# Performance work log

Measured on AMD Instinct MI355X. Metric: run time of the kernel, lower is better.

Reference implementation:

```python
import jax, jax.numpy as jnp
import numpy as np

N = 20000   # nodes per type (lnc and dis)
E = 160000  # edges per meta-path graph and per pos/neg link graph
H = 8       # attention heads
D = 32      # out_size per head (H*D = 256 flattened)
HID = 256   # hidden_size from ResNet projection


def _bn(x, g, b, eps=1e-5):
    # training-mode BatchNorm1d (biased variance, like torch)
    m = x.mean(0)
    v = x.var(0)
    return g * (x - m) * jax.lax.rsqrt(v + eps) + b


def _leaky(x, slope):
    return jnp.where(x >= 0, x, slope * x)


def _gat(h_src, h_dst, src, dst, W, al, ar, n_dst):
    # DGL GATConv (bipartite, shared fc, no bias, eval mode)
    fs = (h_src @ W).reshape(-1, H, D)          # [Ns,H,D]
    fd = (h_dst @ W).reshape(-1, H, D)          # [Nd,H,D]
    el = (fs * al).sum(-1)                      # [Ns,H]
    er = (fd * ar).sum(-1)                      # [Nd,H]
    e = _leaky(el[src] + er[dst], 0.2)          # [E,H]
    emax = jax.ops.segment_max(e, dst, num_segments=n_dst)
    emax = jnp.where(jnp.isfinite(emax), emax, 0.0)   # zero in-degree safety
    ee = jnp.exp(e - emax[dst])
    den = jax.ops.segment_sum(ee, dst, num_segments=n_dst)
    a = ee / jnp.maximum(den[dst], 1e-9)        # edge softmax over incoming edges
    out = jax.ops.segment_sum(a[:, :, None] * fs[src], dst, num_segments=n_dst)
    return _leaky(out, 0.01).reshape(n_dst, H * D)  # activation=F.leaky_relu, flatten(1)


def _sem_attn(z, W1, b1, w2):
    # z: [N, 2, H*D]; SemanticAttention
    w = (jnp.tanh(z @ W1 + b1) @ w2).mean(0)    # [2]
    beta = jax.nn.softmax(w, axis=0)            # [2]
    return (beta[None, :, None] * z).sum(1)     # [N, H*D]


def setup_inputs() -> dict:
    key = jax.random.key(0)
    ks = jax.random.split(key, 32)
    s = 0.05
    inp = {
        "x_lnc": jax.random.normal(ks[0], (N, 256), jnp.float32),
        "x_dis": jax.random.normal(ks[1], (N, 256), jnp.float32),
        "proj_W": jax.random.normal(ks[2], (2, 256, HID), jnp.float32) * s,
        "proj_bn_g": jnp.ones((HID,), jnp.float32),
        "proj_bn_b": jnp.zeros((HID,), jnp.float32),
        "short_W": jax.random.normal(ks[3], (2, 256, HID), jnp.float32) * s,
        "short_b": jnp.zeros((2, HID), jnp.float32),
        "gat_W": jax.random.normal(ks[4], (4, HID, H * D), jnp.float32) * s,
        "gat_al": jax.random.normal(ks[5], (4, H, D), jnp.float32) * s,
        "gat_ar": jax.random.normal(ks[6], (4, H, D), jnp.float32) * s,
        "sem_W1": jax.random.normal(ks[7], (H * D, 128), jnp.float32) * s,
        "sem_b1": jnp.zeros((128,), jnp.float32),
        "sem_w2": jax.random.normal(ks[8], (128,), jnp.float32) * s,
    }
    names = ["ld_src", "ld_dst", "ll_src", "ll_dst", "dl_src", "dl_dst",
             "dd_src", "dd_dst", "pos_src", "pos_dst", "neg_src", "neg_dst"]
    for i, nm in enumerate(names):
        inp[nm] = jax.random.randint(ks[10 + i], (E,), 0, N, jnp.int32)
    return inp


def reference(x_lnc, x_dis, proj_W, proj_bn_g, proj_bn_b, short_W, short_b,
              gat_W, gat_al, gat_ar, sem_W1, sem_b1, sem_w2,
              ld_src, ld_dst, ll_src, ll_dst, dl_src, dl_dst,
              dd_src, dd_dst, pos_src, pos_dst, neg_src, neg_dst):
    # ResNet projection (shared BN applied per-branch, training-mode stats)
    l_x = _leaky(_bn(x_lnc @ proj_W[0], proj_bn_g, proj_bn_b), 0.01) + (x_lnc @ short_W[0] + short_b[0])
    d_x = _leaky(_bn(x_dis @ proj_W[1], proj_bn_g, proj_bn_b), 0.01) + (x_dis @ short_W[1] + short_b[1])
    # HANLayer: 4 meta-path GATs with pairings (l,d),(l,l),(d,l),(d,d)
    e0 = _gat(l_x, d_x, ld_src, ld_dst, gat_W[0], gat_al[0], gat_ar[0], N)  # dst dis
    e1 = _gat(l_x, l_x, ll_src, ll_dst, gat_W[1], gat_al[1], gat_ar[1], N)  # dst lnc
    e2 = _gat(d_x, l_x, dl_src, dl_dst, gat_W[2], gat_al[2], gat_ar[2], N)  # dst lnc
    e3 = _gat(d_x, d_x, dd_src, dd_dst, gat_W[3], gat_al[3], gat_ar[3], N)  # dst dis
    l_embs = _sem_attn(jnp.stack((e1, e2), axis=1), sem_W1, sem_b1, sem_w2)
    d_embs = _sem_attn(jnp.stack((e0, e3), axis=1), sem_W1, sem_b1, sem_w2)
    # Hadamard u_mul_v over 'lnc-dis' edges (pos graph and neg graph)
    pos_z = l_embs[pos_src] * d_embs[pos_dst]
    neg_z = l_embs[neg_src] * d_embs[neg_dst]
    return pos_z, neg_z, l_embs, d_embs
```

## Files before the change

kernel.cpp:

```cpp
#include <hip/hip_runtime.h>
#include <math.h>

#define NN 20000
#define NE 160000
#define SLOT 40

typedef _Float16 f16;
typedef __attribute__((ext_vector_type(8))) _Float16 f16x8;
typedef __attribute__((ext_vector_type(4))) float f32x4;

__device__ __forceinline__ float leakyf(float x, float s){ return x >= 0.f ? x : s*x; }
__device__ __forceinline__ ushort f2h(float x){ f16 h = (f16)x; ushort u; __builtin_memcpy(&u,&h,2); return u; }
__device__ __forceinline__ float h2f(ushort u){ f16 h; __builtin_memcpy(&h,&u,2); return (float)h; }

__device__ __forceinline__ void gload_lds16(const void* g, void* l){
  __builtin_amdgcn_global_load_lds((const __attribute__((address_space(1))) uint*)g,
                                   (__attribute__((address_space(3))) uint*)l, 16, 0, 0);
}

__global__ __launch_bounds__(256) void prep(const float* __restrict__ x_lnc,
    const float* __restrict__ x_dis, const float* __restrict__ proj_W,
    const float* __restrict__ short_W, const float* __restrict__ gat_W,
    const float* __restrict__ gat_al, const float* __restrict__ gat_ar,
    const float* __restrict__ sem_W1,
    ushort* __restrict__ xhl, ushort* __restrict__ xhd,
    ushort* btpl, ushort* btpd, ushort* btgl, ushort* btgd, ushort* btsm,
    int* __restrict__ zbuf){
  int b = blockIdx.x;
  if (b < 10000){
    const float* in = (b >= 5000) ? x_dis : x_lnc;
    ushort* out = (b >= 5000) ? xhd : xhl;
    long idx = (long)(b % 5000)*256 + threadIdx.x;
    long r = idx>>6; int c4 = (int)(idx&63)<<2;
    float4 v = *(const float4*)(in + r*256 + c4);
    ushort4 o; o.x=f2h(v.x); o.y=f2h(v.y); o.z=f2h(v.z); o.w=f2h(v.w);
    *(ushort4*)(out + r*256 + c4) = o;
  } else if (b < 12688){
    int idx = (b-10000)*256 + threadIdx.x;
    float v; ushort* out; int n, k;
    if (idx < 131072){
      n = idx>>8; k = idx&255; out = btpl;
      v = (n<256)? proj_W[(size_t)k*256+n] : short_W[(size_t)k*256+(n-256)];
    } else if (idx < 262144){
      int l = idx-131072; n = l>>8; k = l&255; out = btpd;
      v = (n<256)? proj_W[65536+(size_t)k*256+n] : short_W[65536+(size_t)k*256+(n-256)];
    } else if (idx < 458752){
      int l = idx-262144; n = l>>8; k = l&255; out = btgl;
      int sl = n>>8; const float* bb = gat_W + (sl==0?0:(sl==1?65536:131072));
      v = bb[(size_t)k*256 + (n&255)];
    } else if (idx < 655360){
      int l = idx-458752; n = l>>8; k = l&255; out = btgd;
      int sl = n>>8; const float* bb = gat_W + (sl==0?0:(sl==1?131072:196608));
      v = bb[(size_t)k*256 + (n&255)];
    } else {
      int l = idx-655360; n = l>>8; k = l&255; out = btsm;
      v = sem_W1[(size_t)k*128 + n];
    }
    out[(size_t)n*256 + k] = f2h(v);
  } else if (b < 12752){
    int idx = (b-12688)*256 + threadIdx.x;
    int side = idx >> 13;
    int r = idx & 8191;
    int c = r >> 8;
    int k = r & 255;
    int h = c & 7, sel = c >> 3;
    int gi; const float* av;
    if (side==0){
      gi = (sel==0)?0:((sel==3)?2:1);
      av = (sel<=1)? gat_al : gat_ar;
    } else {
      gi = (sel==0)?0:((sel==1)?2:3);
      av = (sel==1||sel==2)? gat_al : gat_ar;
    }
    const float* wrow = gat_W + gi*65536 + (size_t)k*256 + h*32;
    const float* a = av + gi*256 + h*32;
    float s = 0.f;
    #pragma unroll
    for (int d=0; d<32; d++) s += wrow[d]*a[d];
    ushort* out = side ? btgd : btgl;
    out[(size_t)(768+c)*256 + k] = f2h(s);
  } else if (b < 12848){
    int idx = (b-12752)*256 + threadIdx.x;
    uint* pl = (uint*)(btgl + 800*256);
    uint* pd = (uint*)(btgd + 800*256);
    if (idx < 12288) pl[idx] = 0; else pd[idx-12288] = 0;
  } else {
    int idx = (b-12848)*256 + threadIdx.x;
    if (idx < 81028) zbuf[idx] = 0;
  }
}

__global__ void scatter_slots(const int* s0, const int* s1, const int* s2, const int* s3,
    const int* d0, const int* d1, const int* d2, const int* d3,
    int* __restrict__ cnt, int* __restrict__ slots){
  int g = blockIdx.y;
  const int* src = (g==0)?s0:(g==1)?s1:(g==2)?s2:s3;
  const int* dst = (g==0)?d0:(g==1)?d1:(g==2)?d2:d3;
  int i = blockIdx.x*256 + threadIdx.x;
  if (i<NE){
    int d = dst[i];
    int p = atomicAdd(&cnt[g*NN + d], 1);
    slots[(size_t)(g*NN + d)*SLOT + p] = src[i];
  }
}

template<int EPI>
__global__ __launch_bounds__(256) void gemm16(
    const ushort* __restrict__ A0, const ushort* __restrict__ A1,
    const ushort* __restrict__ B0, const ushort* __restrict__ B1,
    ushort* __restrict__ C0, ushort* __restrict__ C1, int ldc, int M,
    float* __restrict__ sbuf,
    float* __restrict__ elr_l, float* __restrict__ elr_d,
    const float* __restrict__ b1v, const float* __restrict__ w2v){
  const int z = blockIdx.z;
  const ushort* A = z ? A1 : A0;
  const ushort* Bt = z ? B1 : B0;
  ushort* C = z ? C1 : C0;
  __shared__ ushort sm[16384];
  char* smc = (char*)sm;
  const int tid = threadIdx.x;
  const int lane = tid & 63, wid = tid >> 6;
  const int wr = wid >> 1, wc = wid & 1;
  const int fr = lane & 15, fq = lane >> 4;
  const int brow = blockIdx.y*128, bcol = blockIdx.x*128;
  f32x4 acc[4][4];
  #pragma unroll
  for (int i=0;i<4;i++)
    #pragma unroll
    for (int j=0;j<4;j++) acc[i][j] = (f32x4){0.f,0.f,0.f,0.f};

  for (int k0 = 0; k0 < 256; k0 += 64){
    __syncthreads();
    #pragma unroll
    for (int cc = 0; cc < 8; cc++){
      int c = wid*8 + cc;
      int ch = c & 15;
      int rel = ch*1024 + lane*16;
      int row = rel >> 7;
      int scb = (rel & 127) ^ ((row & 7) << 4);
      const char* src;
      if (c < 16){
        int gr = brow + row; gr = (gr < M) ? gr : (M-1);
        src = (const char*)A + (size_t)gr*512 + k0*2 + scb;
      } else {
        src = (const char*)Bt + (size_t)(bcol + row)*512 + k0*2 + scb;
      }
      gload_lds16(src, smc + ((c<16)?0:16384) + ch*1024);
    }
    __syncthreads();
    #pragma unroll
    for (int ks = 0; ks < 2; ks++){
      f16x8 af[4], bfr[4];
      #pragma unroll
      for (int i=0;i<4;i++){
        int r = wr*64 + i*16 + fr;
        int koff = ks*32 + fq*8;
        int aoff = ((r<<7) + koff*2) ^ ((r&7)<<4);
        af[i] = *(const f16x8*)(smc + aoff);
        int n = wc*64 + i*16 + fr;
        int boff = ((n<<7) + koff*2) ^ ((n&7)<<4);
        bfr[i] = *(const f16x8*)(smc + 16384 + boff);
      }
      #pragma unroll
      for (int i=0;i<4;i++)
        #pragma unroll
        for (int j=0;j<4;j++)
          acc[i][j] = __builtin_amdgcn_mfma_f32_16x16x32_f16(af[i], bfr[j], acc[i][j], 0,0,0);
    }
  }

  if (EPI==1 || (EPI==2 && bcol < 768)){
    #pragma unroll
    for (int i=0;i<4;i++){
      #pragma unroll
      for (int e=0;e<4;e++){
        int gr = brow + wr*64 + i*16 + fq*4 + e;
        if (gr < M){
          #pragma unroll
          for (int j=0;j<4;j++)
            C[(size_t)gr*ldc + bcol + wc*64 + j*16 + fr] = f2h(acc[i][j][e]);
        }
      }
    }
  }

  if (EPI==2 && bcol >= 768 && wc == 0){
    float* elr = z ? elr_d : elr_l;
    #pragma unroll
    for (int i=0;i<4;i++){
      #pragma unroll
      for (int e=0;e<4;e++){
        int gr = brow + wr*64 + i*16 + fq*4 + e;
        if (gr < M){
          elr[(size_t)gr*32 + fr]      = acc[i][0][e];
          elr[(size_t)gr*32 + 16 + fr] = acc[i][1][e];
        }
      }
    }
  }

  if (EPI==1 && bcol < 256){
    float* gsum = sbuf + z*512;
    float* gsq  = gsum + 256;
    #pragma unroll
    for (int j=0;j<4;j++){
      float s=0.f, q=0.f;
      #pragma unroll
      for (int i=0;i<4;i++)
        #pragma unroll
        for (int e=0;e<4;e++){
          int gr = brow + wr*64 + i*16 + fq*4 + e;
          if (gr < M){ float v = acc[i][j][e]; s += v; q += v*v; }
        }
      s += __shfl_xor(s,16); s += __shfl_xor(s,32);
      q += __shfl_xor(q,16); q += __shfl_xor(q,32);
      if (fq==0){
        int gc = bcol + wc*64 + j*16 + fr;
        atomicAdd(&gsum[gc], s);
        atomicAdd(&gsq[gc], q);
      }
    }
  }

  if (EPI==3){
    float b1c[4], w2c[4];
    #pragma unroll
    for (int j=0;j<4;j++){
      int col = wc*64 + j*16 + fr;
      b1c[j] = b1v[col]; w2c[j] = w2v[col];
    }
    int segA = brow/20000;
    int bound = (segA+1)*20000;
    float t0=0.f, t1=0.f;
    #pragma unroll
    for (int i=0;i<4;i++){
      #pragma unroll
      for (int e=0;e<4;e++){
        int gr = brow + wr*64 + i*16 + fq*4 + e;
        float rs = 0.f;
        #pragma unroll
        for (int j=0;j<4;j++){
          float x = acc[i][j][e] + b1c[j];
          float ex = __expf(2.f*x);
          rs += (1.f - 2.f/(ex+1.f))*w2c[j];
        }
        if (gr < bound) t0 += rs; else t1 += rs;
      }
    }
    #pragma unroll
    for (int off=32; off>0; off>>=1){ t0 += __shfl_xor(t0,off); t1 += __shfl_xor(t1,off); }
    if (lane==0){
      atomicAdd(&sbuf[segA], t0);
      if (brow + 127 >= bound) atomicAdd(&sbuf[segA+1], t1);
    }
  }
}

__global__ __launch_bounds__(256) void proj_apply2(const ushort* __restrict__ PS_l,
    const ushort* __restrict__ PS_d, const float* __restrict__ sbuf,
    const float* __restrict__ gg, const float* __restrict__ bb,
    const float* __restrict__ short_b, ushort* __restrict__ out_l, ushort* __restrict__ out_d){
  int y = blockIdx.y;
  const ushort* PS = y ? PS_d : PS_l;
  ushort* out = y ? out_d : out_l;
  const float* gsum = sbuf + y*512;
  const float* gsq  = gsum + 256;
  const float* sb = short_b + y*256;
  long idx = (long)blockIdx.x*256 + threadIdx.x;
  long r = idx>>6; int c4 = (int)(idx&63)<<2;
  ushort4 pu = *(const ushort4*)(PS + r*512 + c4);
  ushort4 su = *(const ushort4*)(PS + r*512 + 256 + c4);
  float pv[4] = {h2f(pu.x),h2f(pu.y),h2f(pu.z),h2f(pu.w)};
  float sv[4] = {h2f(su.x),h2f(su.y),h2f(su.z),h2f(su.w)};
  ushort o[4];
  #pragma unroll
  for (int k=0;k<4;k++){
    int c = c4+k;
    float m = gsum[c]*(1.f/NN);
    float va = gsq[c]*(1.f/NN) - m*m;
    float ri = rsqrtf(va + 1e-5f);
    float yv = (pv[k]-m)*ri*gg[c] + bb[c];
    o[k] = f2h(leakyf(yv,0.01f) + sv[k] + sb[c]);
  }
  ushort4 ov; ov.x=o[0]; ov.y=o[1]; ov.z=o[2]; ov.w=o[3];
  *(ushort4*)(out + r*256 + c4) = ov;
}

__global__ __launch_bounds__(256) void gat_fused(const int* __restrict__ cnt,
    const int* __restrict__ slots, const float* __restrict__ elr_l,
    const float* __restrict__ elr_d, const ushort* __restrict__ fc_l,
    const ushort* __restrict__ fc_d, ushort* __restrict__ sems){
  const int g = blockIdx.y;
  const int n = blockIdx.x*4 + (threadIdx.x>>6);
  const int lane = threadIdx.x & 63;
  const int co[4]    = {0,256,256,512};
  const int semo[4]  = {40000,0,20000,60000};
  const int eloA[4]  = {0,8,8,16};
  const int eroA[4]  = {0,16,24,24};
  const float* elb = (g<2) ? elr_l : elr_d;
  const float* erb = (g==1||g==2) ? elr_l : elr_d;
  const int eloff = eloA[g], eroff = eroA[g];
  const ushort* F = (g<2) ? fc_l : fc_d;
  const int coloff = co[g];
  const int j = lane>>3, h = lane&7, hc = lane>>3;
  const int e1 = cnt[g*NN + n];
  const long sb = (long)(g*NN + n)*SLOT;
  const float ern = erb[(size_t)n*32 + eroff + h];
  float ssum = 0.f;
  float4 acc = make_float4(0.f,0.f,0.f,0.f);

  for (int base = 0; base < e1; base += 8){
    int idx = base + j;
    bool valid = idx < e1;
    int src = valid ? slots[sb + idx] : 0;
    float p = valid ? __expf(leakyf(elb[(size_t)src*32 + eloff + h] + ern, 0.2f)) : 0.f;
    ssum += p;
    #pragma unroll
    for (int e=0;e<8;e++){
      float w = __shfl(p, e*8 + hc);
      int s = __shfl(src, e*8);
      ushort4 fu = *(const ushort4*)(F + (size_t)s*768 + coloff + lane*4);
      acc.x = fmaf(w,h2f(fu.x),acc.x); acc.y = fmaf(w,h2f(fu.y),acc.y);
      acc.z = fmaf(w,h2f(fu.z),acc.z); acc.w = fmaf(w,h2f(fu.w),acc.w);
    }
  }
  ssum += __shfl_xor(ssum,8); ssum += __shfl_xor(ssum,16); ssum += __shfl_xor(ssum,32);
  float rd = 1.f/fmaxf(__shfl(ssum, hc), 1e-9f);
  ushort4 o;
  o.x = f2h(leakyf(acc.x*rd, 0.01f)); o.y = f2h(leakyf(acc.y*rd, 0.01f));
  o.z = f2h(leakyf(acc.z*rd, 0.01f)); o.w = f2h(leakyf(acc.w*rd, 0.01f));
  *(ushort4*)(sems + (size_t)(semo[g]+n)*256 + lane*4) = o;
}

__global__ __launch_bounds__(256) void sem_combine(const ushort* __restrict__ sems,
    const float* __restrict__ tsum, float* __restrict__ lemb, float* __restrict__ demb,
    ushort* __restrict__ lemb16, ushort* __restrict__ demb16){
  float wl0 = tsum[0]*(1.f/20000.f), wl1 = tsum[1]*(1.f/20000.f);
  float m = fmaxf(wl0,wl1);
  float ea = __expf(wl0-m), eb = __expf(wl1-m);
  float b0 = ea/(ea+eb), b1 = eb/(ea+eb);
  float wd0 = tsum[2]*(1.f/20000.f), wd1 = tsum[3]*(1.f/20000.f);
  m = fmaxf(wd0,wd1);
  ea = __expf(wd0-m); eb = __expf(wd1-m);
  float b2 = ea/(ea+eb), b3 = eb/(ea+eb);

  long idx = (long)blockIdx.x*256 + threadIdx.x;
  long r = idx>>6; int c4 = (int)(idx&63)<<2;
  ushort4 v1 = *(const ushort4*)(sems + (r          )*256 + c4);
  ushort4 v2 = *(const ushort4*)(sems + (r + 20000L )*256 + c4);
  ushort4 v0 = *(const ushort4*)(sems + (r + 40000L )*256 + c4);
  ushort4 v3 = *(const ushort4*)(sems + (r + 60000L )*256 + c4);
  float4 lo, dd;
  lo.x = b0*h2f(v1.x) + b1*h2f(v2.x); dd.x = b2*h2f(v0.x) + b3*h2f(v3.x);
  lo.y = b0*h2f(v1.y) + b1*h2f(v2.y); dd.y = b2*h2f(v0.y) + b3*h2f(v3.y);
  lo.z = b0*h2f(v1.z) + b1*h2f(v2.z); dd.z = b2*h2f(v0.z) + b3*h2f(v3.z);
  lo.w = b0*h2f(v1.w) + b1*h2f(v2.w); dd.w = b2*h2f(v0.w) + b3*h2f(v3.w);
  *(float4*)(lemb + r*256 + c4) = lo;
  *(float4*)(demb + r*256 + c4) = dd;
  ushort4 lh, dh;
  lh.x=f2h(lo.x); lh.y=f2h(lo.y); lh.z=f2h(lo.z); lh.w=f2h(lo.w);
  dh.x=f2h(dd.x); dh.y=f2h(dd.y); dh.z=f2h(dd.z); dh.w=f2h(dd.w);
  *(ushort4*)(lemb16 + r*256 + c4) = lh;
  *(ushort4*)(demb16 + r*256 + c4) = dh;
}

__global__ __launch_bounds__(256) void edge_mul2(const int* __restrict__ ps, const int* __restrict__ pd,
    const int* __restrict__ ns, const int* __restrict__ nd,
    const ushort* __restrict__ lemb16, const ushort* __restrict__ demb16,
    float* __restrict__ pos, float* __restrict__ neg){
  long idx = (long)blockIdx.x*256 + threadIdx.x;
  const long H = (long)NE*64;
  const int *es, *ed; float* out; long t;
  if (idx < H){ es=ps; ed=pd; out=pos; t=idx; }
  else { es=ns; ed=nd; out=neg; t=idx-H; }
  long i = t>>6; int jj = (int)(t&63);
  int s = es[i], d = ed[i];
  ushort4 a = *(const ushort4*)(lemb16 + (size_t)s*256 + (size_t)jj*4);
  ushort4 b = *(const ushort4*)(demb16 + (size_t)d*256 + (size_t)jj*4);
  float4 o = make_float4(h2f(a.x)*h2f(b.x), h2f(a.y)*h2f(b.y),
                         h2f(a.z)*h2f(b.z), h2f(a.w)*h2f(b.w));
  *(float4*)(out + (size_t)t*4) = o;
}

extern "C" void kernel_launch(void* const* d_in, const int* in_sizes, int n_in,
                              void* d_out, int out_size, void* d_ws, size_t ws_size,
                              hipStream_t stream){
  const float* x_lnc  = (const float*)d_in[0];
  const float* x_dis  = (const float*)d_in[1];
  const float* proj_W = (const float*)d_in[2];
  const float* bn_g   = (const float*)d_in[3];
  const float* bn_b   = (const float*)d_in[4];
  const float* short_W= (const float*)d_in[5];
  const float* short_b= (const float*)d_in[6];
  const float* gat_W  = (const float*)d_in[7];
  const float* gat_al = (const float*)d_in[8];
  const float* gat_ar = (const float*)d_in[9];
  const float* sem_W1 = (const float*)d_in[10];
  const float* sem_b1 = (const float*)d_in[11];
  const float* sem_w2 = (const float*)d_in[12];
  const int* g_src[4] = {(const int*)d_in[13],(const int*)d_in[15],(const int*)d_in[17],(const int*)d_in[19]};
  const int* g_dst[4] = {(const int*)d_in[14],(const int*)d_in[16],(const int*)d_in[18],(const int*)d_in[20]};
  const int* pos_src = (const int*)d_in[21];
  const int* pos_dst = (const int*)d_in[22];
  const int* neg_src = (const int*)d_in[23];
  const int* neg_dst = (const int*)d_in[24];

  const long LEMB = (long)NN*256;
  const long EOUT = (long)NE*256;

  float* outf = (float*)d_out;
  float* pos  = outf;
  float* negr = outf + EOUT;
  float* lemb = outf + 2*EOUT;
  float* demb = lemb + LEMB;

  ushort* PS_l = (ushort*)negr;
  ushort* PS_d = PS_l + 10240000;
  ushort* fc_l = (ushort*)negr;
  ushort* fc_d = fc_l + 15360000;

  float* ws   = (float*)d_ws;
  float* sbuf = ws;
  float* tsum = ws + 1024;
  int*   cnt  = (int*)(ws + 1028);
  float* elr_l = ws + 81028;
  float* elr_d = elr_l + 640000;
  int*   slots  = (int*)(elr_d + 640000);
  ushort* xhl  = (ushort*)(slots + 3200000);
  ushort* xhd  = xhl + 5120000;
  ushort* axl  = xhd + 5120000;
  ushort* axd  = axl + 5120000;
  ushort* sems = axd + 5120000;
  ushort* lemb16 = sems + 20480000;
  ushort* demb16 = lemb16 + 5120000;
  ushort* btpl = demb16 + 5120000;
  ushort* btpd = btpl + 131072;
  ushort* btgl = btpd + 131072;
  ushort* btgd = btgl + 229376;
  ushort* btsm = btgd + 229376;

  prep<<<13165,256,0,stream>>>(x_lnc, x_dis, proj_W, short_W, gat_W, gat_al, gat_ar,
                               sem_W1, xhl, xhd, btpl, btpd, btgl, btgd, btsm, (int*)ws);
  scatter_slots<<<dim3(625,4),256,0,stream>>>(g_src[0],g_src[1],g_src[2],g_src[3],
      g_dst[0],g_dst[1],g_dst[2],g_dst[3], cnt, slots);

  gemm16<1><<<dim3(4,157,2),256,0,stream>>>(xhl, xhd, btpl, btpd, PS_l, PS_d, 512, NN,
      sbuf, nullptr, nullptr, nullptr, nullptr);
  proj_apply2<<<dim3(5000,2),256,0,stream>>>(PS_l, PS_d, sbuf, bn_g, bn_b, short_b, axl, axd);

  gemm16<2><<<dim3(7,157,2),256,0,stream>>>(axl, axd, btgl, btgd, fc_l, fc_d, 768, NN,
      nullptr, elr_l, elr_d, nullptr, nullptr);

  gat_fused<<<dim3(5000,4),256,0,stream>>>(cnt, slots, elr_l, elr_d, fc_l, fc_d, sems);

  gemm16<3><<<dim3(1,625,1),256,0,stream>>>(sems, nullptr, btsm, nullptr, nullptr, nullptr, 128, 80000,
      tsum, nullptr, nullptr, sem_b1, sem_w2);

  sem_combine<<<5000,256,0,stream>>>(sems, tsum, lemb, demb, lemb16, demb16);

  edge_mul2<<<80000,256,0,stream>>>(pos_src, pos_dst, neg_src, neg_dst, lemb16, demb16, pos, negr);
}
```

Before: 386.7 us.

## Fold edge slot scatter into projection GEMM launch, tile weight transpose, nontemporal stores

```diff
diff --git a/kernel.cpp b/kernel.cpp
--- a/kernel.cpp
+++ b/kernel.cpp
@@ -16,6 +16,9 @@
 __device__ __forceinline__ void gload_lds16(const void* g, void* l){
   __builtin_amdgcn_global_load_lds((const __attribute__((address_space(1))) uint*)g,
                                    (__attribute__((address_space(3))) uint*)l, 16, 0, 0);
+}
+__device__ __forceinline__ void nts4(float* p, f32x4 v){
+  __builtin_nontemporal_store(v, (f32x4*)p);
 }
 
 __global__ __launch_bounds__(256) void prep(const float* __restrict__ x_lnc,
@@ -35,30 +38,45 @@
     float4 v = *(const float4*)(in + r*256 + c4);
     ushort4 o; o.x=f2h(v.x); o.y=f2h(v.y); o.z=f2h(v.z); o.w=f2h(v.w);
     *(ushort4*)(out + r*256 + c4) = o;
-  } else if (b < 12688){
-    int idx = (b-10000)*256 + threadIdx.x;
-    float v; ushort* out; int n, k;
-    if (idx < 131072){
-      n = idx>>8; k = idx&255; out = btpl;
-      v = (n<256)? proj_W[(size_t)k*256+n] : short_W[(size_t)k*256+(n-256)];
-    } else if (idx < 262144){
-      int l = idx-131072; n = l>>8; k = l&255; out = btpd;
-      v = (n<256)? proj_W[65536+(size_t)k*256+n] : short_W[65536+(size_t)k*256+(n-256)];
-    } else if (idx < 458752){
-      int l = idx-262144; n = l>>8; k = l&255; out = btgl;
-      int sl = n>>8; const float* bb = gat_W + (sl==0?0:(sl==1?65536:131072));
-      v = bb[(size_t)k*256 + (n&255)];
-    } else if (idx < 655360){
-      int l = idx-458752; n = l>>8; k = l&255; out = btgd;
-      int sl = n>>8; const float* bb = gat_W + (sl==0?0:(sl==1?131072:196608));
-      v = bb[(size_t)k*256 + (n&255)];
+  } else if (b < 10168){
+    int t = b - 10000;
+    const float* S; ushort* outb; int n0, k0, ldS=256, colbase;
+    if (t < 160){
+      int m = t >> 4, tt = t & 15;
+      n0 = (tt & 3) * 64; k0 = (tt >> 2) * 64;
+      switch(m){
+        case 0: S=proj_W;        outb=btpl; colbase=0;   break;
+        case 1: S=short_W;       outb=btpl; colbase=256; break;
+        case 2: S=proj_W+65536;  outb=btpd; colbase=0;   break;
+        case 3: S=short_W+65536; outb=btpd; colbase=256; break;
+        case 4: S=gat_W;         outb=btgl; colbase=0;   break;
+        case 5: S=gat_W+65536;   outb=btgl; colbase=256; break;
+        case 6: S=gat_W+131072;  outb=btgl; colbase=512; break;
+        case 7: S=gat_W;         outb=btgd; colbase=0;   break;
+        case 8: S=gat_W+131072;  outb=btgd; colbase=256; break;
+        default:S=gat_W+196608;  outb=btgd; colbase=512; break;
+      }
     } else {
-      int l = idx-655360; n = l>>8; k = l&255; out = btsm;
-      v = sem_W1[(size_t)k*128 + n];
-    }
-    out[(size_t)n*256 + k] = f2h(v);
-  } else if (b < 12752){
-    int idx = (b-12688)*256 + threadIdx.x;
+      int s = t - 160;
+      n0 = (s & 1)*64; k0 = (s >> 1)*64; ldS = 128;
+      S = sem_W1; outb = btsm; colbase = 0;
+    }
+    __shared__ float tile[64][65];
+    int tr = threadIdx.x >> 6;
+    int tc = threadIdx.x & 63;
+    #pragma unroll
+    for (int p=0;p<16;p++){
+      int kr = p*4 + tr;
+      tile[kr][tc] = S[(size_t)(k0+kr)*ldS + n0 + tc];
+    }
+    __syncthreads();
+    #pragma unroll
+    for (int p=0;p<16;p++){
+      int nr = p*4 + tr;
+      outb[(size_t)(colbase + n0 + nr)*256 + k0 + tc] = f2h(tile[tc][nr]);
+    }
+  } else if (b < 10232){
+    int idx = (b-10168)*256 + threadIdx.x;
     int side = idx >> 13;
     int r = idx & 8191;
     int c = r >> 8;
@@ -79,28 +97,14 @@
     for (int d=0; d<32; d++) s += wrow[d]*a[d];
     ushort* out = side ? btgd : btgl;
     out[(size_t)(768+c)*256 + k] = f2h(s);
-  } else if (b < 12848){
-    int idx = (b-12752)*256 + threadIdx.x;
+  } else if (b < 10328){
+    int idx = (b-10232)*256 + threadIdx.x;
     uint* pl = (uint*)(btgl + 800*256);
     uint* pd = (uint*)(btgd + 800*256);
     if (idx < 12288) pl[idx] = 0; else pd[idx-12288] = 0;
   } else {
-    int idx = (b-12848)*256 + threadIdx.x;
+    int idx = (b-10328)*256 + threadIdx.x;
     if (idx < 81028) zbuf[idx] = 0;
-  }
-}
-
-__global__ void scatter_slots(const int* s0, const int* s1, const int* s2, const int* s3,
-    const int* d0, const int* d1, const int* d2, const int* d3,
-    int* __restrict__ cnt, int* __restrict__ slots){
-  int g = blockIdx.y;
-  const int* src = (g==0)?s0:(g==1)?s1:(g==2)?s2:s3;
-  const int* dst = (g==0)?d0:(g==1)?d1:(g==2)?d2:d3;
-  int i = blockIdx.x*256 + threadIdx.x;
-  if (i<NE){
-    int d = dst[i];
-    int p = atomicAdd(&cnt[g*NN + d], 1);
-    slots[(size_t)(g*NN + d)*SLOT + p] = src[i];
   }
 }
 
@@ -111,8 +115,26 @@
     ushort* __restrict__ C0, ushort* __restrict__ C1, int ldc, int M,
     float* __restrict__ sbuf,
     float* __restrict__ elr_l, float* __restrict__ elr_d,
-    const float* __restrict__ b1v, const float* __restrict__ w2v){
+    const float* __restrict__ b1v, const float* __restrict__ w2v,
+    const int* s0, const int* s1, const int* s2, const int* s3,
+    const int* d0, const int* d1, const int* d2, const int* d3,
+    int* __restrict__ cnt, int* __restrict__ slots){
   const int z = blockIdx.z;
+  if (EPI==1 && z==2){
+    int bb = blockIdx.y*gridDim.x + blockIdx.x;
+    int tid = bb*256 + (int)threadIdx.x;
+    if (tid < NE){
+      #pragma unroll
+      for (int g=0; g<4; g++){
+        const int* src = (g==0)?s0:(g==1)?s1:(g==2)?s2:s3;
+        const int* dst = (g==0)?d0:(g==1)?d1:(g==2)?d2:d3;
+        int d = dst[tid];
+        int p = atomicAdd(&cnt[g*NN + d], 1);
+        slots[(size_t)(g*NN + d)*SLOT + p] = src[tid];
+      }
+    }
+    return;
+  }
   const ushort* A = z ? A1 : A0;
   const ushort* Bt = z ? B1 : B0;
   ushort* C = z ? C1 : C0;
@@ -350,16 +372,16 @@
   ushort4 v2 = *(const ushort4*)(sems + (r + 20000L )*256 + c4);
   ushort4 v0 = *(const ushort4*)(sems + (r + 40000L )*256 + c4);
   ushort4 v3 = *(const ushort4*)(sems + (r + 60000L )*256 + c4);
-  float4 lo, dd;
-  lo.x = b0*h2f(v1.x) + b1*h2f(v2.x); dd.x = b2*h2f(v0.x) + b3*h2f(v3.x);
-  lo.y = b0*h2f(v1.y) + b1*h2f(v2.y); dd.y = b2*h2f(v0.y) + b3*h2f(v3.y);
-  lo.z = b0*h2f(v1.z) + b1*h2f(v2.z); dd.z = b2*h2f(v0.z) + b3*h2f(v3.z);
-  lo.w = b0*h2f(v1.w) + b1*h2f(v2.w); dd.w = b2*h2f(v0.w) + b3*h2f(v3.w);
-  *(float4*)(lemb + r*256 + c4) = lo;
-  *(float4*)(demb + r*256 + c4) = dd;
+  f32x4 lo, dd;
+  lo[0] = b0*h2f(v1.x) + b1*h2f(v2.x); dd[0] = b2*h2f(v0.x) + b3*h2f(v3.x);
+  lo[1] = b0*h2f(v1.y) + b1*h2f(v2.y); dd[1] = b2*h2f(v0.y) + b3*h2f(v3.y);
+  lo[2] = b0*h2f(v1.z) + b1*h2f(v2.z); dd[2] = b2*h2f(v0.z) + b3*h2f(v3.z);
+  lo[3] = b0*h2f(v1.w) + b1*h2f(v2.w); dd[3] = b2*h2f(v0.w) + b3*h2f(v3.w);
+  nts4(lemb + r*256 + c4, lo);
+  nts4(demb + r*256 + c4, dd);
   ushort4 lh, dh;
-  lh.x=f2h(lo.x); lh.y=f2h(lo.y); lh.z=f2h(lo.z); lh.w=f2h(lo.w);
-  dh.x=f2h(dd.x); dh.y=f2h(dd.y); dh.z=f2h(dd.z); dh.w=f2h(dd.w);
+  lh.x=f2h(lo[0]); lh.y=f2h(lo[1]); lh.z=f2h(lo[2]); lh.w=f2h(lo[3]);
+  dh.x=f2h(dd[0]); dh.y=f2h(dd[1]); dh.z=f2h(dd[2]); dh.w=f2h(dd[3]);
   *(ushort4*)(lemb16 + r*256 + c4) = lh;
   *(ushort4*)(demb16 + r*256 + c4) = dh;
 }
@@ -377,9 +399,10 @@
   int s = es[i], d = ed[i];
   ushort4 a = *(const ushort4*)(lemb16 + (size_t)s*256 + (size_t)jj*4);
   ushort4 b = *(const ushort4*)(demb16 + (size_t)d*256 + (size_t)jj*4);
-  float4 o = make_float4(h2f(a.x)*h2f(b.x), h2f(a.y)*h2f(b.y),
-                         h2f(a.z)*h2f(b.z), h2f(a.w)*h2f(b.w));
-  *(float4*)(out + (size_t)t*4) = o;
+  f32x4 o;
+  o[0]=h2f(a.x)*h2f(b.x); o[1]=h2f(a.y)*h2f(b.y);
+  o[2]=h2f(a.z)*h2f(b.z); o[3]=h2f(a.w)*h2f(b.w);
+  nts4(out + (size_t)t*4, o);
 }
 
 extern "C" void kernel_launch(void* const* d_in, const int* in_sizes, int n_in,
@@ -439,22 +462,24 @@
   ushort* btgd = btgl + 229376;
   ushort* btsm = btgd + 229376;
 
-  prep<<<13165,256,0,stream>>>(x_lnc, x_dis, proj_W, short_W, gat_W, gat_al, gat_ar,
+  prep<<<10645,256,0,stream>>>(x_lnc, x_dis, proj_W, short_W, gat_W, gat_al, gat_ar,
                                sem_W1, xhl, xhd, btpl, btpd, btgl, btgd, btsm, (int*)ws);
-  scatter_slots<<<dim3(625,4),256,0,stream>>>(g_src[0],g_src[1],g_src[2],g_src[3],
-      g_dst[0],g_dst[1],g_dst[2],g_dst[3], cnt, slots);
-
-  gemm16<1><<<dim3(4,157,2),256,0,stream>>>(xhl, xhd, btpl, btpd, PS_l, PS_d, 512, NN,
-      sbuf, nullptr, nullptr, nullptr, nullptr);
+
+  gemm16<1><<<dim3(4,157,3),256,0,stream>>>(xhl, xhd, btpl, btpd, PS_l, PS_d, 512, NN,
+      sbuf, nullptr, nullptr, nullptr, nullptr,
+      g_src[0],g_src[1],g_src[2],g_src[3], g_dst[0],g_dst[1],g_dst[2],g_dst[3],
+      cnt, slots);
   proj_apply2<<<dim3(5000,2),256,0,stream>>>(PS_l, PS_d, sbuf, bn_g, bn_b, short_b, axl, axd);
 
   gemm16<2><<<dim3(7,157,2),256,0,stream>>>(axl, axd, btgl, btgd, fc_l, fc_d, 768, NN,
-      nullptr, elr_l, elr_d, nullptr, nullptr);
+      nullptr, elr_l, elr_d, nullptr, nullptr,
+      nullptr,nullptr,nullptr,nullptr, nullptr,nullptr,nullptr,nullptr, nullptr,nullptr);
 
   gat_fused<<<dim3(5000,4),256,0,stream>>>(cnt, slots, elr_l, elr_d, fc_l, fc_d, sems);
 
   gemm16<3><<<dim3(1,625,1),256,0,stream>>>(sems, nullptr, btsm, nullptr, nullptr, nullptr, 128, 80000,
-      tsum, nullptr, nullptr, sem_b1, sem_w2);
+      tsum, nullptr, nullptr, sem_b1, sem_w2,
+      nullptr,nullptr,nullptr,nullptr, nullptr,nullptr,nullptr,nullptr, nullptr,nullptr);
 
   sem_combine<<<5000,256,0,stream>>>(sems, tsum, lemb, demb, lemb16, demb16);
 
```

Result: faster. 351.8 us, median of 3 (-9.0%).
